# Performance work log

Hardware: AMD Instinct MI355X
Metric: run time of the kernel (lower is better)

The kernel has to match this reference:

```python
import jax, jax.numpy as jnp
import numpy as np

EMBED_DIM = 512
U_EMBED = 6
NUM_HEADS = 8
HEAD_DIM = EMBED_DIM // NUM_HEADS
SCALE = HEAD_DIM ** -0.5
BS, N = 8, 1024


def setup_inputs() -> dict:
    key = jax.random.key(0)
    ks = jax.random.split(key, 9)
    x = jax.random.normal(ks[0], (BS, N, EMBED_DIM), dtype=jnp.float32)
    u = jax.random.normal(ks[1], (BS, U_EMBED, N, N), dtype=jnp.float32)
    umask = jax.random.randint(ks[2], (BS, N, N, 1), 0, 2).astype(bool)
    s = EMBED_DIM ** -0.5
    Wq = jax.random.normal(ks[3], (EMBED_DIM, EMBED_DIM), dtype=jnp.float32) * s
    Wk = jax.random.normal(ks[4], (EMBED_DIM, EMBED_DIM), dtype=jnp.float32) * s
    Wv = jax.random.normal(ks[5], (EMBED_DIM, EMBED_DIM), dtype=jnp.float32) * s
    Wu = jax.random.normal(ks[6], (NUM_HEADS, U_EMBED), dtype=jnp.float32) * (U_EMBED ** -0.5)
    bu = jnp.zeros((NUM_HEADS,), dtype=jnp.float32)
    Wo = jax.random.normal(ks[7], (EMBED_DIM, EMBED_DIM), dtype=jnp.float32) * s
    bo = jnp.zeros((EMBED_DIM,), dtype=jnp.float32)
    return {"x": x, "u": u, "umask": umask, "Wq": Wq, "Wk": Wk, "Wv": Wv,
            "Wu": Wu, "bu": bu, "Wo": Wo, "bo": bo}


def reference(x, u, umask, Wq, Wk, Wv, Wu, bu, Wo, bo):
    bs, n, _ = x.shape
    # projections (torch Linear: y = x @ W.T)
    Q = (x @ Wq.T).reshape(bs, n, NUM_HEADS, HEAD_DIM)
    K = (x @ Wk.T).reshape(bs, n, NUM_HEADS, HEAD_DIM)
    V = (x @ Wv.T).reshape(bs, n, NUM_HEADS, HEAD_DIM)
    # scores: [bs, H, N, N]
    scores = jnp.einsum('bqhd,bkhd->bhqk', Q, K) * SCALE
    # 1x1 conv bias: [bs, u_embed, N, N] -> [bs, H, N, N]
    ub = jnp.einsum('bunm,hu->bhnm', u, Wu) + bu[None, :, None, None]
    # umask: [bs, N, N, 1] -> transpose(3,1) -> [bs, 1, N, N]
    m = jnp.transpose(umask, (0, 3, 2, 1))
    ub = jnp.where(m, -jnp.inf, ub)
    scores = scores + ub
    attn = jax.nn.softmax(scores, axis=-1)
    ctx = jnp.einsum('bhqk,bkhd->bqhd', attn, V).reshape(bs, n, EMBED_DIM)
    out = ctx @ Wo.T + bo
    return out, attn
```

## Files before the change

kernel.cpp:

```cpp
#include <hip/hip_runtime.h>
#include <hip/hip_bf16.h>
#include <math.h>

#define BSZ 8
#define SEQ 1024
#define EMB 512
#define NH 8
#define HD 64
#define UE 6
#define QKSCALE 0.125f

typedef unsigned short u16;
typedef short bf16x8 __attribute__((ext_vector_type(8)));
typedef float f32x4 __attribute__((ext_vector_type(4)));
typedef unsigned short ushort4_t __attribute__((ext_vector_type(4)));

__device__ __forceinline__ u16 f2bf(float f) {
  unsigned u = __float_as_uint(f);
  unsigned r = (u + 0x7fffu + ((u >> 16) & 1u)) >> 16;
  return (u16)r;
}
__device__ __forceinline__ void f2hl(float f, u16& hi, u16& lo) {
  hi = f2bf(f);
  float fh = __uint_as_float(((unsigned)hi) << 16);
  lo = f2bf(f - fh);
}
#define F2HL_V(fv, hv, lv, idx)            \
  {                                        \
    u16 _h, _l;                            \
    f2hl((fv), _h, _l);                    \
    (hv)[idx] = (short)_h;                 \
    (lv)[idx] = (short)_l;                 \
  }
__device__ __forceinline__ f32x4 mfma_bf16(bf16x8 a, bf16x8 b, f32x4 c) {
  return __builtin_amdgcn_mfma_f32_16x16x32_bf16(a, b, c, 0, 0, 0);
}

__global__ __launch_bounds__(256) void split_kernel(const float* __restrict__ src,
                                                    u16* __restrict__ hi, u16* __restrict__ lo, int n4) {
  int i = blockIdx.x * 256 + threadIdx.x;
  if (i >= n4) return;
  float4 v = ((const float4*)src)[i];
  ushort4_t h, l;
  F2HL_V(v.x, h, l, 0); F2HL_V(v.y, h, l, 1);
  F2HL_V(v.z, h, l, 2); F2HL_V(v.w, h, l, 3);
  ((ushort4_t*)hi)[i] = h;
  ((ushort4_t*)lo)[i] = l;
}

__global__ __launch_bounds__(256, 2) void qkv_mfma_kernel(
    const float* __restrict__ x, const u16* __restrict__ Wsp,
    u16* __restrict__ Qhi, u16* __restrict__ Qlo,
    u16* __restrict__ Khi, u16* __restrict__ Klo, u16* __restrict__ Vt) {
  const int mt = blockIdx.x, h = blockIdx.y, wsel = blockIdx.z;
  const int m0 = mt * 64, c0 = h * 64;
  const u16* __restrict__ WH = Wsp + (size_t)wsel * 524288;
  const u16* __restrict__ WL = WH + 262144;
  __shared__ u16 AH[64][40], AL[64][40], BH[64][40], BL[64][40];
  __shared__ u16 vout[64][69];
  const int t = threadIdx.x, w = t >> 6, l = t & 63;
  const int wr = (w >> 1) * 32, wc = (w & 1) * 32;
  f32x4 acc[2][2] = {};
  const int srow = t >> 2;
  for (int e0 = 0; e0 < EMB; e0 += 32) {
    {
      const int c = (t & 3) * 8;
      float4 v0 = *(const float4*)&x[(size_t)(m0 + srow) * EMB + e0 + c];
      float4 v1 = *(const float4*)&x[(size_t)(m0 + srow) * EMB + e0 + c + 4];
      ushort4_t h0, l0, h1, l1;
      F2HL_V(v0.x, h0, l0, 0); F2HL_V(v0.y, h0, l0, 1); F2HL_V(v0.z, h0, l0, 2); F2HL_V(v0.w, h0, l0, 3);
      F2HL_V(v1.x, h1, l1, 0); F2HL_V(v1.y, h1, l1, 1); F2HL_V(v1.z, h1, l1, 2); F2HL_V(v1.w, h1, l1, 3);
      *(ushort4_t*)&AH[srow][c] = h0; *(ushort4_t*)&AH[srow][c + 4] = h1;
      *(ushort4_t*)&AL[srow][c] = l0; *(ushort4_t*)&AL[srow][c + 4] = l1;
      *(bf16x8*)&BH[srow][c] = *(const bf16x8*)&WH[(size_t)(c0 + srow) * EMB + e0 + c];
      *(bf16x8*)&BL[srow][c] = *(const bf16x8*)&WL[(size_t)(c0 + srow) * EMB + e0 + c];
    }
    __syncthreads();
    const int ar = l & 15, ach = (l >> 4) << 3;
    bf16x8 ah0 = *(bf16x8*)&AH[wr + ar][ach],      ah1 = *(bf16x8*)&AH[wr + 16 + ar][ach];
    bf16x8 al0 = *(bf16x8*)&AL[wr + ar][ach],      al1 = *(bf16x8*)&AL[wr + 16 + ar][ach];
    bf16x8 bh0 = *(bf16x8*)&BH[wc + ar][ach],      bh1 = *(bf16x8*)&BH[wc + 16 + ar][ach];
    bf16x8 bl0 = *(bf16x8*)&BL[wc + ar][ach],      bl1 = *(bf16x8*)&BL[wc + 16 + ar][ach];
    acc[0][0] = mfma_bf16(ah0, bh0, acc[0][0]); acc[0][0] = mfma_bf16(ah0, bl0, acc[0][0]); acc[0][0] = mfma_bf16(al0, bh0, acc[0][0]);
    acc[0][1] = mfma_bf16(ah0, bh1, acc[0][1]); acc[0][1] = mfma_bf16(ah0, bl1, acc[0][1]); acc[0][1] = mfma_bf16(al0, bh1, acc[0][1]);
    acc[1][0] = mfma_bf16(ah1, bh0, acc[1][0]); acc[1][0] = mfma_bf16(ah1, bl0, acc[1][0]); acc[1][0] = mfma_bf16(al1, bh0, acc[1][0]);
    acc[1][1] = mfma_bf16(ah1, bh1, acc[1][1]); acc[1][1] = mfma_bf16(ah1, bl1, acc[1][1]); acc[1][1] = mfma_bf16(al1, bh1, acc[1][1]);
    __syncthreads();
  }
  const int bb = m0 >> 10, n0 = m0 & 1023;
  if (wsel < 2) {
    u16* __restrict__ OH = wsel ? Khi : Qhi;
    u16* __restrict__ OL = wsel ? Klo : Qlo;
#pragma unroll
    for (int i = 0; i < 2; ++i)
#pragma unroll
      for (int j = 0; j < 2; ++j) {
        const int col = wc + 16 * j + (l & 15);
#pragma unroll
        for (int r = 0; r < 4; ++r) {
          const int n = n0 + wr + 16 * i + ((l >> 4) << 2) + r;
          size_t o = ((size_t)(bb * NH + h) * SEQ + n) * HD + col;
          u16 hi, lo; f2hl(acc[i][j][r], hi, lo);
          OH[o] = hi; OL[o] = lo;
        }
      }
  } else {
#pragma unroll
    for (int i = 0; i < 2; ++i)
#pragma unroll
      for (int j = 0; j < 2; ++j) {
        const int col = wc + 16 * j + (l & 15);
#pragma unroll
        for (int r = 0; r < 4; ++r)
          vout[wr + 16 * i + ((l >> 4) << 2) + r][col] = f2bf(acc[i][j][r]);
      }
    __syncthreads();
    const int d = t >> 2, nch = (t & 3) * 16;
    bf16x8 o0, o1;
#pragma unroll
    for (int i = 0; i < 8; ++i) o0[i] = (short)vout[nch + i][d];
#pragma unroll
    for (int i = 0; i < 8; ++i) o1[i] = (short)vout[nch + 8 + i][d];
    size_t dst = ((size_t)(bb * NH + h) * HD + d) * SEQ + n0 + nch;
    *(bf16x8*)&Vt[dst] = o0;
    *(bf16x8*)&Vt[dst + 8] = o1;
  }
}

__global__ __launch_bounds__(256, 2) void scores_kernel(
    const u16* __restrict__ Qhi, const u16* __restrict__ Qlo,
    const u16* __restrict__ Khi, const u16* __restrict__ Klo,
    const float* __restrict__ u, const int* __restrict__ umask,
    const float* __restrict__ Wu, const float* __restrict__ bu,
    float* __restrict__ attn) {
  const int kt = blockIdx.x, qt = blockIdx.y, b = blockIdx.z;
  const int q0 = qt * 64, k0 = kt * 64;
  __shared__ u16 KsH[64][72], KsL[64][72];
  __shared__ unsigned char ms[64][68];
  const int t = threadIdx.x, w = t >> 6, l = t & 63;
  const int qb = 16 * w + ((l >> 4) << 2);
  const int kl = l & 15;

#pragma unroll
  for (int r = 0; r < 16; ++r) {
    int idx = r * 256 + t; int k = idx >> 6, q = idx & 63;
    ms[k][q] = (unsigned char)(umask[((size_t)b * SEQ + k0 + k) * SEQ + q0 + q] != 0);
  }

  unsigned upk[UE][4][2];
  {
    const float* ubase = u + ((size_t)b * UE * SEQ + q0 + qb) * SEQ + k0 + kl;
#pragma unroll
    for (int uu = 0; uu < UE; ++uu)
#pragma unroll
      for (int tt = 0; tt < 4; ++tt)
#pragma unroll
        for (int p = 0; p < 2; ++p) {
          const float* up = ubase + (size_t)uu * SEQ * SEQ + (size_t)(2 * p) * SEQ + 16 * tt;
          float f0 = up[0], f1 = up[SEQ];
          upk[uu][tt][p] = (unsigned)f2bf(f0) | ((unsigned)f2bf(f1) << 16);
        }
  }

  const int krow_s = t >> 2, kc_s = (t & 3) * 16;
  bf16x8 kpre0, kpre1, kpre2, kpre3;
  {
    const u16* kp = Khi + ((size_t)(b * NH) * SEQ + k0 + krow_s) * HD + kc_s;
    const u16* kq = Klo + ((size_t)(b * NH) * SEQ + k0 + krow_s) * HD + kc_s;
    kpre0 = *(const bf16x8*)kp; kpre1 = *(const bf16x8*)(kp + 8);
    kpre2 = *(const bf16x8*)kq; kpre3 = *(const bf16x8*)(kq + 8);
  }

  for (int h = 0; h < NH; ++h) {
    const int bh = b * NH + h;
    __syncthreads();
    *(bf16x8*)&KsH[krow_s][kc_s] = kpre0;
    *(bf16x8*)&KsH[krow_s][kc_s + 8] = kpre1;
    *(bf16x8*)&KsL[krow_s][kc_s] = kpre2;
    *(bf16x8*)&KsL[krow_s][kc_s + 8] = kpre3;
    if (h < NH - 1) {
      const u16* kp = Khi + ((size_t)(bh + 1) * SEQ + k0 + krow_s) * HD + kc_s;
      const u16* kq = Klo + ((size_t)(bh + 1) * SEQ + k0 + krow_s) * HD + kc_s;
      kpre0 = *(const bf16x8*)kp; kpre1 = *(const bf16x8*)(kp + 8);
      kpre2 = *(const bf16x8*)kq; kpre3 = *(const bf16x8*)(kq + 8);
    }
    __syncthreads();

    const u16* qp = Qhi + ((size_t)bh * SEQ + q0 + 16 * w + (l & 15)) * HD + ((l >> 4) << 3);
    const u16* ql = Qlo + ((size_t)bh * SEQ + q0 + 16 * w + (l & 15)) * HD + ((l >> 4) << 3);
    bf16x8 qh0 = *(const bf16x8*)qp, qh1 = *(const bf16x8*)(qp + 32);
    bf16x8 ql0 = *(const bf16x8*)ql, ql1 = *(const bf16x8*)(ql + 32);
    float wu_[UE];
#pragma unroll
    for (int uu = 0; uu < UE; ++uu) wu_[uu] = Wu[h * UE + uu];
    const float bub = bu[h];
    float* abase = attn + ((size_t)bh * SEQ + q0 + qb) * SEQ + k0 + kl;
#pragma unroll
    for (int tt = 0; tt < 4; ++tt) {
      const int krow = tt * 16 + (l & 15), kch = (l >> 4) << 3;
      bf16x8 kh0 = *(bf16x8*)&KsH[krow][kch], kh1 = *(bf16x8*)&KsH[krow][kch + 32];
      bf16x8 kl0 = *(bf16x8*)&KsL[krow][kch], kl1 = *(bf16x8*)&KsL[krow][kch + 32];
      f32x4 acc = {0.f, 0.f, 0.f, 0.f};
      acc = mfma_bf16(qh0, kh0, acc); acc = mfma_bf16(qh1, kh1, acc);
      acc = mfma_bf16(qh0, kl0, acc); acc = mfma_bf16(qh1, kl1, acc);
      acc = mfma_bf16(ql0, kh0, acc); acc = mfma_bf16(ql1, kh1, acc);
#pragma unroll
      for (int p = 0; p < 2; ++p) {
        float ubx = bub, uby = bub;
#pragma unroll
        for (int uu = 0; uu < UE; ++uu) {
          unsigned pk = upk[uu][tt][p];
          float flo = __uint_as_float(pk << 16);
          float fhi = __uint_as_float(pk & 0xffff0000u);
          ubx = fmaf(wu_[uu], flo, ubx);
          uby = fmaf(wu_[uu], fhi, uby);
        }
#pragma unroll
        for (int e = 0; e < 2; ++e) {
          const int r = 2 * p + e;
          float v = acc[r] * QKSCALE + (e ? uby : ubx);
          if (ms[tt * 16 + kl][qb + r]) v = -INFINITY;
          abase[(size_t)r * SEQ + tt * 16] = v;
        }
      }
    }
  }
}

__global__ __launch_bounds__(256, 2) void pv_softmax_kernel(
    float* __restrict__ attn, const u16* __restrict__ Vt,
    u16* __restrict__ ctx_hi, u16* __restrict__ ctx_lo) {
  const int qt = blockIdx.x, bh = blockIdx.y;
  const int q0 = qt * 64;
  __shared__ u16 Pl[64][72], Vs[64][72];
  const int t = threadIdx.x, w = t >> 6, l = t & 63;
  const int row = t >> 2, cc = (t & 3) * 16;
  float* arow = attn + ((size_t)bh * SEQ + q0 + row) * SEQ + cc;

  float M = -INFINITY, S = 0.f;
  for (int k0 = 0; k0 < SEQ; k0 += 64) {
    float4 v0 = *(const float4*)(arow + k0);
    float4 v1 = *(const float4*)(arow + k0 + 4);
    float4 v2 = *(const float4*)(arow + k0 + 8);
    float4 v3 = *(const float4*)(arow + k0 + 12);
    float tm = fmaxf(fmaxf(fmaxf(v0.x, v0.y), fmaxf(v0.z, v0.w)),
                     fmaxf(fmaxf(v1.x, v1.y), fmaxf(v1.z, v1.w)));
    tm = fmaxf(tm, fmaxf(fmaxf(fmaxf(v2.x, v2.y), fmaxf(v2.z, v2.w)),
                         fmaxf(fmaxf(v3.x, v3.y), fmaxf(v3.z, v3.w))));
    if (tm > M) { S *= __expf(M - tm); M = tm; }
    S += __expf(v0.x - M) + __expf(v0.y - M) + __expf(v0.z - M) + __expf(v0.w - M)
       + __expf(v1.x - M) + __expf(v1.y - M) + __expf(v1.z - M) + __expf(v1.w - M)
       + __expf(v2.x - M) + __expf(v2.y - M) + __expf(v2.z - M) + __expf(v2.w - M)
       + __expf(v3.x - M) + __expf(v3.y - M) + __expf(v3.z - M) + __expf(v3.w - M);
  }
#pragma unroll
  for (int o = 1; o <= 2; o <<= 1) {
    float Mo = __shfl_xor(M, o), So = __shfl_xor(S, o);
    float Mn = fmaxf(M, Mo);
    S = S * __expf(M - Mn) + So * __expf(Mo - Mn);
    M = Mn;
  }
  const float inv = 1.0f / S;

  const int wr = (w >> 1) * 32, wc = (w & 1) * 32;
  f32x4 acc[2][2] = {};
  for (int k0 = 0; k0 < SEQ; k0 += 64) {
    bf16x8 p0, p1;
#pragma unroll
    for (int c4 = 0; c4 < 4; ++c4) {
      float4 v = *(const float4*)(arow + k0 + 4 * c4);
      float4 p;
      p.x = __expf(v.x - M) * inv; p.y = __expf(v.y - M) * inv;
      p.z = __expf(v.z - M) * inv; p.w = __expf(v.w - M) * inv;
      *(float4*)(arow + k0 + 4 * c4) = p;
      if (c4 < 2) {
        p0[4 * c4 + 0] = (short)f2bf(p.x); p0[4 * c4 + 1] = (short)f2bf(p.y);
        p0[4 * c4 + 2] = (short)f2bf(p.z); p0[4 * c4 + 3] = (short)f2bf(p.w);
      } else {
        p1[4 * (c4 - 2) + 0] = (short)f2bf(p.x); p1[4 * (c4 - 2) + 1] = (short)f2bf(p.y);
        p1[4 * (c4 - 2) + 2] = (short)f2bf(p.z); p1[4 * (c4 - 2) + 3] = (short)f2bf(p.w);
      }
    }
    *(bf16x8*)&Pl[row][cc] = p0;
    *(bf16x8*)&Pl[row][cc + 8] = p1;
    {
      const u16* vp = Vt + ((size_t)bh * HD + row) * SEQ + k0 + cc;
      *(bf16x8*)&Vs[row][cc] = *(const bf16x8*)vp;
      *(bf16x8*)&Vs[row][cc + 8] = *(const bf16x8*)(vp + 8);
    }
    __syncthreads();
#pragma unroll
    for (int kb = 0; kb < 2; ++kb) {
      const int kch = kb * 32 + ((l >> 4) << 3);
      bf16x8 a0 = *(bf16x8*)&Pl[wr + (l & 15)][kch];
      bf16x8 a1 = *(bf16x8*)&Pl[wr + 16 + (l & 15)][kch];
      bf16x8 b0 = *(bf16x8*)&Vs[wc + (l & 15)][kch];
      bf16x8 b1 = *(bf16x8*)&Vs[wc + 16 + (l & 15)][kch];
      acc[0][0] = mfma_bf16(a0, b0, acc[0][0]);
      acc[0][1] = mfma_bf16(a0, b1, acc[0][1]);
      acc[1][0] = mfma_bf16(a1, b0, acc[1][0]);
      acc[1][1] = mfma_bf16(a1, b1, acc[1][1]);
    }
    __syncthreads();
  }
  const int b = bh >> 3, h = bh & 7;
#pragma unroll
  for (int i = 0; i < 2; ++i)
#pragma unroll
    for (int j = 0; j < 2; ++j) {
      const int d = h * HD + wc + 16 * j + (l & 15);
#pragma unroll
      for (int r = 0; r < 4; ++r) {
        const int q = q0 + wr + 16 * i + ((l >> 4) << 2) + r;
        size_t o = ((size_t)(b * SEQ + q)) * EMB + d;
        u16 hi, lo; f2hl(acc[i][j][r], hi, lo);
        ctx_hi[o] = hi; ctx_lo[o] = lo;
      }
    }
}

__global__ __launch_bounds__(256, 2) void oproj_kernel(
    const u16* __restrict__ ctx_hi, const u16* __restrict__ ctx_lo,
    const u16* __restrict__ WoH, const u16* __restrict__ WoL,
    const float* __restrict__ bo, float* __restrict__ out) {
  const int mt = blockIdx.x, ct = blockIdx.y;
  const int m0 = mt * 64, c0 = ct * 64;
  __shared__ u16 AH[64][40], AL[64][40], BH[64][40], BL[64][40];
  const int t = threadIdx.x, w = t >> 6, l = t & 63;
  const int wr = (w >> 1) * 32, wc = (w & 1) * 32;
  f32x4 acc[2][2] = {};
  const int srow = t >> 2, sc = (t & 3) * 8;
  for (int e0 = 0; e0 < EMB; e0 += 32) {
    *(bf16x8*)&AH[srow][sc] = *(const bf16x8*)&ctx_hi[(size_t)(m0 + srow) * EMB + e0 + sc];
    *(bf16x8*)&AL[srow][sc] = *(const bf16x8*)&ctx_lo[(size_t)(m0 + srow) * EMB + e0 + sc];
    *(bf16x8*)&BH[srow][sc] = *(const bf16x8*)&WoH[(size_t)(c0 + srow) * EMB + e0 + sc];
    *(bf16x8*)&BL[srow][sc] = *(const bf16x8*)&WoL[(size_t)(c0 + srow) * EMB + e0 + sc];
    __syncthreads();
    const int ar = l & 15, ach = (l >> 4) << 3;
    bf16x8 ah0 = *(bf16x8*)&AH[wr + ar][ach],      ah1 = *(bf16x8*)&AH[wr + 16 + ar][ach];
    bf16x8 al0 = *(bf16x8*)&AL[wr + ar][ach],      al1 = *(bf16x8*)&AL[wr + 16 + ar][ach];
    bf16x8 bh0 = *(bf16x8*)&BH[wc + ar][ach],      bh1 = *(bf16x8*)&BH[wc + 16 + ar][ach];
    bf16x8 bl0 = *(bf16x8*)&BL[wc + ar][ach],      bl1 = *(bf16x8*)&BL[wc + 16 + ar][ach];
    acc[0][0] = mfma_bf16(ah0, bh0, acc[0][0]); acc[0][0] = mfma_bf16(ah0, bl0, acc[0][0]); acc[0][0] = mfma_bf16(al0, bh0, acc[0][0]);
    acc[0][1] = mfma_bf16(ah0, bh1, acc[0][1]); acc[0][1] = mfma_bf16(ah0, bl1, acc[0][1]); acc[0][1] = mfma_bf16(al0, bh1, acc[0][1]);
    acc[1][0] = mfma_bf16(ah1, bh0, acc[1][0]); acc[1][0] = mfma_bf16(ah1, bl0, acc[1][0]); acc[1][0] = mfma_bf16(al1, bh0, acc[1][0]);
    acc[1][1] = mfma_bf16(ah1, bh1, acc[1][1]); acc[1][1] = mfma_bf16(ah1, bl1, acc[1][1]); acc[1][1] = mfma_bf16(al1, bh1, acc[1][1]);
    __syncthreads();
  }
#pragma unroll
  for (int i = 0; i < 2; ++i)
#pragma unroll
    for (int j = 0; j < 2; ++j) {
      const int col = c0 + wc + 16 * j + (l & 15);
      const float bias = bo[col];
#pragma unroll
      for (int r = 0; r < 4; ++r) {
        const int m = m0 + wr + 16 * i + ((l >> 4) << 2) + r;
        out[(size_t)m * EMB + col] = acc[i][j][r] + bias;
      }
    }
}

extern "C" void kernel_launch(void* const* d_in, const int* in_sizes, int n_in,
                              void* d_out, int out_size, void* d_ws, size_t ws_size,
                              hipStream_t stream) {
  const float* x = (const float*)d_in[0];
  const float* u = (const float*)d_in[1];
  const int* umask = (const int*)d_in[2];
  const float* Wq = (const float*)d_in[3];
  const float* Wk = (const float*)d_in[4];
  const float* Wv = (const float*)d_in[5];
  const float* Wu = (const float*)d_in[6];
  const float* bu = (const float*)d_in[7];
  const float* Wo = (const float*)d_in[8];
  const float* bo = (const float*)d_in[9];

  float* out = (float*)d_out;
  float* attn = out + (size_t)BSZ * SEQ * EMB;

  const size_t per = (size_t)BSZ * NH * SEQ * HD;
  u16* ws = (u16*)d_ws;
  u16* Qhi = ws;
  u16* Qlo = Qhi + per;
  u16* Khi = Qlo + per;
  u16* Klo = Khi + per;
  u16* Vt = Klo + per;
  u16* ctx_hi = Vt + per;
  u16* ctx_lo = ctx_hi + per;
  u16* Wsp = ctx_lo + per;

  const int wn4 = 262144 / 4;
  split_kernel<<<dim3(wn4 / 256), 256, 0, stream>>>(Wq, Wsp + 0 * 524288, Wsp + 0 * 524288 + 262144, wn4);
  split_kernel<<<dim3(wn4 / 256), 256, 0, stream>>>(Wk, Wsp + 1 * 524288, Wsp + 1 * 524288 + 262144, wn4);
  split_kernel<<<dim3(wn4 / 256), 256, 0, stream>>>(Wv, Wsp + 2 * 524288, Wsp + 2 * 524288 + 262144, wn4);
  split_kernel<<<dim3(wn4 / 256), 256, 0, stream>>>(Wo, Wsp + 3 * 524288, Wsp + 3 * 524288 + 262144, wn4);

  qkv_mfma_kernel<<<dim3(128, 8, 3), 256, 0, stream>>>(x, Wsp, Qhi, Qlo, Khi, Klo, Vt);
  scores_kernel<<<dim3(16, 16, 8), 256, 0, stream>>>(Qhi, Qlo, Khi, Klo, u, umask, Wu, bu, attn);
  pv_softmax_kernel<<<dim3(16, 64), 256, 0, stream>>>(attn, Vt, ctx_hi, ctx_lo);
  oproj_kernel<<<dim3(128, 8), 256, 0, stream>>>(ctx_hi, ctx_lo, Wsp + 3 * 524288, Wsp + 3 * 524288 + 262144, bo, out);
}
```

Before: 427.3 us.

## Compute per-tile softmax max/sum in scores kernel, drop stats pass, prefetch PV loads

The scores kernel now reduces each 64-wide key tile to a (max, sum-exp) pair per query row and writes these pairs to workspace. The PV kernel merges the 16 pairs per row instead of re-reading the full fp32 attention row to compute softmax statistics, which removes one full pass over the large attn matrix. The PV loop also register-prefetches the next attn and V tiles. Context is now stored as a single bf16 instead of a hi/lo split, cutting one MFMA per step and one ctx buffer in the output projection at some precision cost.

```diff
diff --git a/kernel.cpp b/kernel.cpp
--- a/kernel.cpp
+++ b/kernel.cpp
@@ -132,7 +132,7 @@
     const u16* __restrict__ Khi, const u16* __restrict__ Klo,
     const float* __restrict__ u, const int* __restrict__ umask,
     const float* __restrict__ Wu, const float* __restrict__ bu,
-    float* __restrict__ attn) {
+    float* __restrict__ attn, float2* __restrict__ pairs) {
   const int kt = blockIdx.x, qt = blockIdx.y, b = blockIdx.z;
   const int q0 = qt * 64, k0 = kt * 64;
   __shared__ u16 KsH[64][72], KsL[64][72];
@@ -195,6 +195,8 @@
     for (int uu = 0; uu < UE; ++uu) wu_[uu] = Wu[h * UE + uu];
     const float bub = bu[h];
     float* abase = attn + ((size_t)bh * SEQ + q0 + qb) * SEQ + k0 + kl;
+
+    float sv[4][4];
 #pragma unroll
     for (int tt = 0; tt < 4; ++tt) {
       const int krow = tt * 16 + (l & 15), kch = (l >> 4) << 3;
@@ -215,21 +217,33 @@
           ubx = fmaf(wu_[uu], flo, ubx);
           uby = fmaf(wu_[uu], fhi, uby);
         }
-#pragma unroll
-        for (int e = 0; e < 2; ++e) {
-          const int r = 2 * p + e;
-          float v = acc[r] * QKSCALE + (e ? uby : ubx);
-          if (ms[tt * 16 + kl][qb + r]) v = -INFINITY;
-          abase[(size_t)r * SEQ + tt * 16] = v;
-        }
+        sv[2 * p + 0][tt] = ms[tt * 16 + kl][qb + 2 * p + 0] ? -INFINITY : acc[2 * p + 0] * QKSCALE + ubx;
+        sv[2 * p + 1][tt] = ms[tt * 16 + kl][qb + 2 * p + 1] ? -INFINITY : acc[2 * p + 1] * QKSCALE + uby;
       }
+    }
+#pragma unroll
+    for (int r = 0; r < 4; ++r)
+#pragma unroll
+      for (int tt = 0; tt < 4; ++tt)
+        abase[(size_t)r * SEQ + tt * 16] = sv[r][tt];
+#pragma unroll
+    for (int r = 0; r < 4; ++r) {
+      float m = fmaxf(fmaxf(sv[r][0], sv[r][1]), fmaxf(sv[r][2], sv[r][3]));
+#pragma unroll
+      for (int o = 1; o <= 8; o <<= 1) m = fmaxf(m, __shfl_xor(m, o));
+      float s = __expf(sv[r][0] - m) + __expf(sv[r][1] - m) +
+                __expf(sv[r][2] - m) + __expf(sv[r][3] - m);
+#pragma unroll
+      for (int o = 1; o <= 8; o <<= 1) s += __shfl_xor(s, o);
+      if (kl == 0)
+        pairs[((size_t)bh * SEQ + q0 + qb + r) * 16 + kt] = make_float2(m, s);
     }
   }
 }
 
 __global__ __launch_bounds__(256, 2) void pv_softmax_kernel(
     float* __restrict__ attn, const u16* __restrict__ Vt,
-    u16* __restrict__ ctx_hi, u16* __restrict__ ctx_lo) {
+    const float2* __restrict__ pairs, u16* __restrict__ ctx) {
   const int qt = blockIdx.x, bh = blockIdx.y;
   const int q0 = qt * 64;
   __shared__ u16 Pl[64][72], Vs[64][72];
@@ -238,55 +252,64 @@
   float* arow = attn + ((size_t)bh * SEQ + q0 + row) * SEQ + cc;
 
   float M = -INFINITY, S = 0.f;
-  for (int k0 = 0; k0 < SEQ; k0 += 64) {
-    float4 v0 = *(const float4*)(arow + k0);
-    float4 v1 = *(const float4*)(arow + k0 + 4);
-    float4 v2 = *(const float4*)(arow + k0 + 8);
-    float4 v3 = *(const float4*)(arow + k0 + 12);
-    float tm = fmaxf(fmaxf(fmaxf(v0.x, v0.y), fmaxf(v0.z, v0.w)),
-                     fmaxf(fmaxf(v1.x, v1.y), fmaxf(v1.z, v1.w)));
-    tm = fmaxf(tm, fmaxf(fmaxf(fmaxf(v2.x, v2.y), fmaxf(v2.z, v2.w)),
-                         fmaxf(fmaxf(v3.x, v3.y), fmaxf(v3.z, v3.w))));
-    if (tm > M) { S *= __expf(M - tm); M = tm; }
-    S += __expf(v0.x - M) + __expf(v0.y - M) + __expf(v0.z - M) + __expf(v0.w - M)
-       + __expf(v1.x - M) + __expf(v1.y - M) + __expf(v1.z - M) + __expf(v1.w - M)
-       + __expf(v2.x - M) + __expf(v2.y - M) + __expf(v2.z - M) + __expf(v2.w - M)
-       + __expf(v3.x - M) + __expf(v3.y - M) + __expf(v3.z - M) + __expf(v3.w - M);
-  }
-#pragma unroll
-  for (int o = 1; o <= 2; o <<= 1) {
-    float Mo = __shfl_xor(M, o), So = __shfl_xor(S, o);
-    float Mn = fmaxf(M, Mo);
-    S = S * __expf(M - Mn) + So * __expf(Mo - Mn);
-    M = Mn;
+  {
+    const float2* pp = pairs + ((size_t)bh * SEQ + q0 + row) * 16 + (t & 3) * 4;
+#pragma unroll
+    for (int j = 0; j < 4; ++j) {
+      float2 c = pp[j];
+      float Mn = fmaxf(M, c.x);
+      S = S * __expf(M - Mn) + c.y * __expf(c.x - Mn);
+      M = Mn;
+    }
+#pragma unroll
+    for (int o = 1; o <= 2; o <<= 1) {
+      float Mo = __shfl_xor(M, o), So = __shfl_xor(S, o);
+      float Mn = fmaxf(M, Mo);
+      S = S * __expf(M - Mn) + So * __expf(Mo - Mn);
+      M = Mn;
+    }
   }
   const float inv = 1.0f / S;
 
   const int wr = (w >> 1) * 32, wc = (w & 1) * 32;
   f32x4 acc[2][2] = {};
+  float4 va0 = *(const float4*)(arow + 0), va1 = *(const float4*)(arow + 4);
+  float4 va2 = *(const float4*)(arow + 8), va3 = *(const float4*)(arow + 12);
+  const u16* vrow = Vt + ((size_t)bh * HD + row) * SEQ + cc;
+  bf16x8 vb0 = *(const bf16x8*)vrow, vb1 = *(const bf16x8*)(vrow + 8);
+
   for (int k0 = 0; k0 < SEQ; k0 += 64) {
     bf16x8 p0, p1;
-#pragma unroll
-    for (int c4 = 0; c4 < 4; ++c4) {
-      float4 v = *(const float4*)(arow + k0 + 4 * c4);
-      float4 p;
-      p.x = __expf(v.x - M) * inv; p.y = __expf(v.y - M) * inv;
-      p.z = __expf(v.z - M) * inv; p.w = __expf(v.w - M) * inv;
-      *(float4*)(arow + k0 + 4 * c4) = p;
-      if (c4 < 2) {
-        p0[4 * c4 + 0] = (short)f2bf(p.x); p0[4 * c4 + 1] = (short)f2bf(p.y);
-        p0[4 * c4 + 2] = (short)f2bf(p.z); p0[4 * c4 + 3] = (short)f2bf(p.w);
-      } else {
-        p1[4 * (c4 - 2) + 0] = (short)f2bf(p.x); p1[4 * (c4 - 2) + 1] = (short)f2bf(p.y);
-        p1[4 * (c4 - 2) + 2] = (short)f2bf(p.z); p1[4 * (c4 - 2) + 3] = (short)f2bf(p.w);
-      }
-    }
+    float4 p;
+    p.x = __expf(va0.x - M) * inv; p.y = __expf(va0.y - M) * inv;
+    p.z = __expf(va0.z - M) * inv; p.w = __expf(va0.w - M) * inv;
+    *(float4*)(arow + k0 + 0) = p;
+    p0[0] = (short)f2bf(p.x); p0[1] = (short)f2bf(p.y); p0[2] = (short)f2bf(p.z); p0[3] = (short)f2bf(p.w);
+    p.x = __expf(va1.x - M) * inv; p.y = __expf(va1.y - M) * inv;
+    p.z = __expf(va1.z - M) * inv; p.w = __expf(va1.w - M) * inv;
+    *(float4*)(arow + k0 + 4) = p;
+    p0[4] = (short)f2bf(p.x); p0[5] = (short)f2bf(p.y); p0[6] = (short)f2bf(p.z); p0[7] = (short)f2bf(p.w);
+    p.x = __expf(va2.x - M) * inv; p.y = __expf(va2.y - M) * inv;
+    p.z = __expf(va2.z - M) * inv; p.w = __expf(va2.w - M) * inv;
+    *(float4*)(arow + k0 + 8) = p;
+    p1[0] = (short)f2bf(p.x); p1[1] = (short)f2bf(p.y); p1[2] = (short)f2bf(p.z); p1[3] = (short)f2bf(p.w);
+    p.x = __expf(va3.x - M) * inv; p.y = __expf(va3.y - M) * inv;
+    p.z = __expf(va3.z - M) * inv; p.w = __expf(va3.w - M) * inv;
+    *(float4*)(arow + k0 + 12) = p;
+    p1[4] = (short)f2bf(p.x); p1[5] = (short)f2bf(p.y); p1[6] = (short)f2bf(p.z); p1[7] = (short)f2bf(p.w);
+
     *(bf16x8*)&Pl[row][cc] = p0;
     *(bf16x8*)&Pl[row][cc + 8] = p1;
-    {
-      const u16* vp = Vt + ((size_t)bh * HD + row) * SEQ + k0 + cc;
-      *(bf16x8*)&Vs[row][cc] = *(const bf16x8*)vp;
-      *(bf16x8*)&Vs[row][cc + 8] = *(const bf16x8*)(vp + 8);
+    *(bf16x8*)&Vs[row][cc] = vb0;
+    *(bf16x8*)&Vs[row][cc + 8] = vb1;
+
+    if (k0 + 64 < SEQ) {
+      va0 = *(const float4*)(arow + k0 + 64);
+      va1 = *(const float4*)(arow + k0 + 68);
+      va2 = *(const float4*)(arow + k0 + 72);
+      va3 = *(const float4*)(arow + k0 + 76);
+      vb0 = *(const bf16x8*)(vrow + k0 + 64);
+      vb1 = *(const bf16x8*)(vrow + k0 + 72);
     }
     __syncthreads();
 #pragma unroll
@@ -312,39 +335,35 @@
 #pragma unroll
       for (int r = 0; r < 4; ++r) {
         const int q = q0 + wr + 16 * i + ((l >> 4) << 2) + r;
-        size_t o = ((size_t)(b * SEQ + q)) * EMB + d;
-        u16 hi, lo; f2hl(acc[i][j][r], hi, lo);
-        ctx_hi[o] = hi; ctx_lo[o] = lo;
+        ctx[((size_t)(b * SEQ + q)) * EMB + d] = f2bf(acc[i][j][r]);
       }
     }
 }
 
 __global__ __launch_bounds__(256, 2) void oproj_kernel(
-    const u16* __restrict__ ctx_hi, const u16* __restrict__ ctx_lo,
+    const u16* __restrict__ ctx,
     const u16* __restrict__ WoH, const u16* __restrict__ WoL,
     const float* __restrict__ bo, float* __restrict__ out) {
   const int mt = blockIdx.x, ct = blockIdx.y;
   const int m0 = mt * 64, c0 = ct * 64;
-  __shared__ u16 AH[64][40], AL[64][40], BH[64][40], BL[64][40];
+  __shared__ u16 AH[64][40], BH[64][40], BL[64][40];
   const int t = threadIdx.x, w = t >> 6, l = t & 63;
   const int wr = (w >> 1) * 32, wc = (w & 1) * 32;
   f32x4 acc[2][2] = {};
   const int srow = t >> 2, sc = (t & 3) * 8;
   for (int e0 = 0; e0 < EMB; e0 += 32) {
-    *(bf16x8*)&AH[srow][sc] = *(const bf16x8*)&ctx_hi[(size_t)(m0 + srow) * EMB + e0 + sc];
-    *(bf16x8*)&AL[srow][sc] = *(const bf16x8*)&ctx_lo[(size_t)(m0 + srow) * EMB + e0 + sc];
+    *(bf16x8*)&AH[srow][sc] = *(const bf16x8*)&ctx[(size_t)(m0 + srow) * EMB + e0 + sc];
     *(bf16x8*)&BH[srow][sc] = *(const bf16x8*)&WoH[(size_t)(c0 + srow) * EMB + e0 + sc];
     *(bf16x8*)&BL[srow][sc] = *(const bf16x8*)&WoL[(size_t)(c0 + srow) * EMB + e0 + sc];
     __syncthreads();
     const int ar = l & 15, ach = (l >> 4) << 3;
     bf16x8 ah0 = *(bf16x8*)&AH[wr + ar][ach],      ah1 = *(bf16x8*)&AH[wr + 16 + ar][ach];
-    bf16x8 al0 = *(bf16x8*)&AL[wr + ar][ach],      al1 = *(bf16x8*)&AL[wr + 16 + ar][ach];
     bf16x8 bh0 = *(bf16x8*)&BH[wc + ar][ach],      bh1 = *(bf16x8*)&BH[wc + 16 + ar][ach];
     bf16x8 bl0 = *(bf16x8*)&BL[wc + ar][ach],      bl1 = *(bf16x8*)&BL[wc + 16 + ar][ach];
-    acc[0][0] = mfma_bf16(ah0, bh0, acc[0][0]); acc[0][0] = mfma_bf16(ah0, bl0, acc[0][0]); acc[0][0] = mfma_bf16(al0, bh0, acc[0][0]);
-    acc[0][1] = mfma_bf16(ah0, bh1, acc[0][1]); acc[0][1] = mfma_bf16(ah0, bl1, acc[0][1]); acc[0][1] = mfma_bf16(al0, bh1, acc[0][1]);
-    acc[1][0] = mfma_bf16(ah1, bh0, acc[1][0]); acc[1][0] = mfma_bf16(ah1, bl0, acc[1][0]); acc[1][0] = mfma_bf16(al1, bh0, acc[1][0]);
-    acc[1][1] = mfma_bf16(ah1, bh1, acc[1][1]); acc[1][1] = mfma_bf16(ah1, bl1, acc[1][1]); acc[1][1] = mfma_bf16(al1, bh1, acc[1][1]);
+    acc[0][0] = mfma_bf16(ah0, bh0, acc[0][0]); acc[0][0] = mfma_bf16(ah0, bl0, acc[0][0]);
+    acc[0][1] = mfma_bf16(ah0, bh1, acc[0][1]); acc[0][1] = mfma_bf16(ah0, bl1, acc[0][1]);
+    acc[1][0] = mfma_bf16(ah1, bh0, acc[1][0]); acc[1][0] = mfma_bf16(ah1, bl0, acc[1][0]);
+    acc[1][1] = mfma_bf16(ah1, bh1, acc[1][1]); acc[1][1] = mfma_bf16(ah1, bl1, acc[1][1]);
     __syncthreads();
   }
 #pragma unroll
@@ -385,9 +404,9 @@
   u16* Khi = Qlo + per;
   u16* Klo = Khi + per;
   u16* Vt = Klo + per;
-  u16* ctx_hi = Vt + per;
-  u16* ctx_lo = ctx_hi + per;
-  u16* Wsp = ctx_lo + per;
+  u16* ctx = Vt + per;
+  float2* pairs = (float2*)(ctx + per);
+  u16* Wsp = (u16*)((char*)pairs + (size_t)BSZ * NH * SEQ * 16 * sizeof(float2));
 
   const int wn4 = 262144 / 4;
   split_kernel<<<dim3(wn4 / 256), 256, 0, stream>>>(Wq, Wsp + 0 * 524288, Wsp + 0 * 524288 + 262144, wn4);
@@ -396,7 +415,7 @@
   split_kernel<<<dim3(wn4 / 256), 256, 0, stream>>>(Wo, Wsp + 3 * 524288, Wsp + 3 * 524288 + 262144, wn4);
 
   qkv_mfma_kernel<<<dim3(128, 8, 3), 256, 0, stream>>>(x, Wsp, Qhi, Qlo, Khi, Klo, Vt);
-  scores_kernel<<<dim3(16, 16, 8), 256, 0, stream>>>(Qhi, Qlo, Khi, Klo, u, umask, Wu, bu, attn);
-  pv_softmax_kernel<<<dim3(16, 64), 256, 0, stream>>>(attn, Vt, ctx_hi, ctx_lo);
-  oproj_kernel<<<dim3(128, 8), 256, 0, stream>>>(ctx_hi, ctx_lo, Wsp + 3 * 524288, Wsp + 3 * 524288 + 262144, bo, out);
-}
+  scores_kernel<<<dim3(16, 16, 8), 256, 0, stream>>>(Qhi, Qlo, Khi, Klo, u, umask, Wu, bu, attn, pairs);
+  pv_softmax_kernel<<<dim3(16, 64), 256, 0, stream>>>(attn, Vt, pairs, ctx);
+  oproj_kernel<<<dim3(128, 8), 256, 0, stream>>>(ctx, Wsp + 3 * 524288, Wsp + 3 * 524288 + 262144, bo, out);
+}
```

Result: no change. 421.7 us (-1.3%).
